# Performance work log

Hardware: AMD Instinct MI355X
Metric: run time of the kernel (lower is better)

The kernel has to match this reference:

```python
import jax, jax.numpy as jnp
import numpy as np

N_CLASSES = 12
IMG_SIZE = 512
BATCH = 8

CURV_MAX = jnp.array([1.2261, 1.1558, 1.1161, 1.1195, 2.7202, 2.3714,
                      1.7055, 3.2717, 2.6716, 5.0418, 0.4293], dtype=jnp.float32)


def setup_inputs() -> dict:
    key = jax.random.key(0)
    soft_anatomy = jax.random.normal(key, (BATCH, N_CLASSES, IMG_SIZE, IMG_SIZE), dtype=jnp.float32)
    return {"soft_anatomy": soft_anatomy}


def reference(soft_anatomy):
    nc1 = N_CLASSES - 1  # 11 layer channels
    pred_mask = soft_anatomy[:, :nc1]                      # [B, 11, H, W]
    sm = jax.nn.softmax(pred_mask, axis=2)                 # softmax over height (dim 2)
    lsm = jax.nn.log_softmax(pred_mask, axis=2)
    B, C, H, W = sm.shape

    # position mask: row index broadcast over width/channels
    pos = jnp.arange(H, dtype=sm.dtype)[None, None, :, None]  # [1,1,H,1]

    # expected layer position per column: [B, 11, W]
    layer_positions = jnp.sum(sm * pos, axis=2)

    # std deviations around layer positions: [B, 11, W]
    std_deviations = jnp.sqrt(
        jnp.sum(sm * (pos - layer_positions[:, :, None, :]) ** 2, axis=2))

    # topology violations between adjacent layers: [B, 10, W]
    topology_violations = jax.nn.relu(layer_positions[:, :-1] - layer_positions[:, 1:])

    # neighbour (continuity) diff along width: [B, 11, W-1]
    continuity_violations = jnp.abs(
        (jnp.roll(layer_positions, 1, axis=2) - layer_positions)[..., 1:])

    # curvature via depthwise conv1d with sobel [-1,0..0,1] and laplace [1,0..0,-2,0..0,1]
    # (kernel length 11, replicate pad 5 -> same width). torch conv1d is cross-correlation:
    #   first[w]  = -x[w] + x[w+10]
    #   second[w] =  x[w] - 2*x[w+5] + x[w+10]
    PAD = 5
    lpp = jnp.pad(layer_positions, ((0, 0), (0, 0), (PAD, PAD)), mode='edge')
    first_order = lpp[..., 10:] - lpp[..., :-10]
    second_order = lpp[..., :-10] - 2.0 * lpp[..., 5:-5] + lpp[..., 10:]
    curvature = second_order / jnp.power(1.0 + first_order ** 2, 1.5)
    curvature_diffs = jnp.abs(curvature) - CURV_MAX[None, :, None]  # curv_max broadcast over W

    # topological_engine_1d: new[i] = max(new[i-1], lp[i]) == cumulative max over class dim
    correct_layer_positions = jax.lax.cummax(layer_positions, axis=1)

    # cumulative mask: ones channel + cumsum over height -> [B, 12, H, W]
    cum = jnp.cumsum(sm, axis=2)
    ones = jnp.ones((B, 1, H, W), dtype=sm.dtype)
    cm = jnp.concatenate([ones, cum], axis=1)

    # topological_engine_2d: y[idx] = relu(c[idx] + y[idx-1] - 1), idx = 2..n_classes-1
    def step(carry, c):
        y = jax.nn.relu(c + carry - 1.0)
        return y, y

    _, ys = jax.lax.scan(step, cm[:, 1], jnp.moveaxis(cm[:, 2:], 1, 0))
    top_correct = jnp.concatenate([cm[:, :2], jnp.moveaxis(ys, 0, 1)], axis=1)  # [B,12,H,W]

    # separate_masks: forward diff in place; last channel unchanged
    clean_masks = jnp.concatenate(
        [top_correct[:, :-1] - top_correct[:, 1:], top_correct[:, -1:]], axis=1)

    return (lsm, correct_layer_positions, clean_masks,
            std_deviations, topology_violations, continuity_violations, curvature_diffs)
```

## Files before the change

kernel.cpp:

```cpp
#include <hip/hip_runtime.h>

#define BB 8
#define NC 12
#define NC1 11
#define HH 512
#define WW 512
#define NCH 32
#define HC 16
#define NBC (BB*NC1)

static constexpr size_t CH = (size_t)HH * WW;

static constexpr size_t OFF_LSM   = 0;
static constexpr size_t OFF_CLP   = (size_t)BB * NC1 * CH;
static constexpr size_t OFF_CLEAN = OFF_CLP + (size_t)BB * NC1 * WW;
static constexpr size_t OFF_STD   = OFF_CLEAN + (size_t)BB * NC * CH;
static constexpr size_t OFF_TOPO  = OFF_STD + (size_t)BB * NC1 * WW;
static constexpr size_t OFF_CONT  = OFF_TOPO + (size_t)BB * (NC1 - 1) * WW;
static constexpr size_t OFF_CURV  = OFF_CONT + (size_t)BB * NC1 * (WW - 1);

static constexpr size_t WS_E    = 0;
static constexpr size_t WS_P    = (size_t)NBC * NCH * WW;
static constexpr size_t WS_Q    = 2 * WS_P;
static constexpr size_t WS_INV  = 3 * WS_P;
static constexpr size_t WS_LOG  = WS_INV + (size_t)NBC * WW;
static constexpr size_t WS_LP   = WS_LOG + (size_t)NBC * WW;

__global__ __launch_bounds__(512) void k1_partials(const float* __restrict__ in,
                                                   float* __restrict__ ws) {
    const int w4 = threadIdx.x & 127;
    const int cg = threadIdx.x >> 7;
    const int chunk = blockIdx.x * 4 + cg;
    const int bc = blockIdx.y;
    const int b = bc / NC1, c = bc % NC1;

    const float* p = in + ((size_t)(b * NC + c) * HH + (size_t)chunk * HC) * WW + 4 * w4;
    float4 E = make_float4(0.f, 0.f, 0.f, 0.f);
    float4 P = E, Q = E;
#pragma unroll
    for (int i = 0; i < HC; ++i) {
        const float4 x = *(const float4*)(p + (size_t)i * WW);
        const float h = (float)(chunk * HC + i);
        const float ex = expf(x.x), ey = expf(x.y), ez = expf(x.z), ew = expf(x.w);
        E.x += ex; E.y += ey; E.z += ez; E.w += ew;
        P.x += h * ex; P.y += h * ey; P.z += h * ez; P.w += h * ew;
        Q.x += h * h * ex; Q.y += h * h * ey; Q.z += h * h * ez; Q.w += h * h * ew;
    }
    const size_t o = ((size_t)bc * NCH + chunk) * WW + 4 * w4;
    *(float4*)(ws + WS_E + o) = E;
    *(float4*)(ws + WS_P + o) = P;
    *(float4*)(ws + WS_Q + o) = Q;
}

__global__ __launch_bounds__(512) void k2_reduce(float* __restrict__ ws,
                                                 float* __restrict__ out) {
    const int w = threadIdx.x & 127;
    const int q = threadIdx.x >> 7;
    const int wt = blockIdx.x;
    const int bc = blockIdx.y;
    const int wg = wt * 128 + w;

    __shared__ float sE[4][128], sP[4][128], sQ[4][128];

    const size_t base = (size_t)bc * NCH * WW + wg;
    float e[8];
    float Es = 0.f, Ps = 0.f, Qs = 0.f;
#pragma unroll
    for (int k = 0; k < 8; ++k) {
        const int ch = q * 8 + k;
        e[k] = ws[WS_E + base + (size_t)ch * WW];
        Es += e[k];
        Ps += ws[WS_P + base + (size_t)ch * WW];
        Qs += ws[WS_Q + base + (size_t)ch * WW];
    }
    sE[q][w] = Es; sP[q][w] = Ps; sQ[q][w] = Qs;
    __syncthreads();

    const float S = sE[0][w] + sE[1][w] + sE[2][w] + sE[3][w];
    const float inv = 1.f / S;
    float pre = 0.f;
    for (int q2 = 0; q2 < q; ++q2) pre += sE[q2][w];
#pragma unroll
    for (int k = 0; k < 8; ++k) {
        const int ch = q * 8 + k;
        ws[WS_E + base + (size_t)ch * WW] = pre * inv;
        pre += e[k];
    }
    if (q == 0) {
        const float P = sP[0][w] + sP[1][w] + sP[2][w] + sP[3][w];
        const float Q = sQ[0][w] + sQ[1][w] + sQ[2][w] + sQ[3][w];
        const float lp = P * inv;
        float var = Q * inv - lp * lp;
        if (var < 0.f) var = 0.f;
        const size_t o = (size_t)bc * WW + wg;
        ws[WS_INV + o] = inv;
        ws[WS_LOG + o] = logf(S);
        ws[WS_LP + o]  = lp;
        out[OFF_STD + o] = sqrtf(var);
    }
}

__global__ __launch_bounds__(256) void k4_main(const float* __restrict__ in,
                                               const float* __restrict__ ws,
                                               float* __restrict__ out) {
    const int t = threadIdx.x;
    const int wh = blockIdx.x, chunk = blockIdx.y, b = blockIdx.z;
    const int w = wh * 256 + t;

    float cum[NC1], inv[NC1], lgs[NC1];
#pragma unroll
    for (int c = 0; c < NC1; ++c) {
        const size_t bc = (size_t)(b * NC1 + c);
        cum[c] = ws[WS_E + (bc * NCH + chunk) * WW + w];
        inv[c] = ws[WS_INV + bc * WW + w];
        lgs[c] = ws[WS_LOG + bc * WW + w];
    }

    const float* ip = in + (size_t)b * NC * CH + (size_t)(chunk * HC) * WW + w;
    float* lsm = out + OFF_LSM + (size_t)b * NC1 * CH + (size_t)(chunk * HC) * WW + w;
    float* cln = out + OFF_CLEAN + (size_t)b * NC * CH + (size_t)(chunk * HC) * WW + w;

    for (int i = 0; i < HC; ++i) {
        const size_t ho = (size_t)i * WW;
        float x[NC1];
#pragma unroll
        for (int c = 0; c < NC1; ++c)
            x[c] = ip[(size_t)c * CH + ho];
#pragma unroll
        for (int c = 0; c < NC1; ++c) {
            cum[c] += expf(x[c]) * inv[c];
            lsm[(size_t)c * CH + ho] = x[c] - lgs[c];
        }
        float tc = cum[0];
        cln[ho] = 1.f - tc;
#pragma unroll
        for (int k = 1; k < NC1; ++k) {
            const float t2 = fmaxf(cum[k] + tc - 1.f, 0.f);
            cln[(size_t)k * CH + ho] = tc - t2;
            tc = t2;
        }
        cln[(size_t)NC1 * CH + ho] = tc;
    }

    if (chunk != 0) return;
    const float CM[NC1] = {1.2261f, 1.1558f, 1.1161f, 1.1195f, 2.7202f, 2.3714f,
                           1.7055f, 3.2717f, 2.6716f, 5.0418f, 0.4293f};
    const float* lp = ws + WS_LP;
    const int wm = (w - 5 < 0) ? 0 : w - 5;
    const int wp = (w + 5 > WW - 1) ? WW - 1 : w + 5;
    float m = 0.f, prev = 0.f;
    for (int c = 0; c < NC1; ++c) {
        const size_t rb = (size_t)(b * NC1 + c) * WW;
        const float lv = lp[rb + w];
        m = (c == 0) ? lv : fmaxf(m, lv);
        out[OFF_CLP + rb + w] = m;
        if (c > 0)
            out[OFF_TOPO + (size_t)(b * (NC1 - 1) + (c - 1)) * WW + w] = fmaxf(prev - lv, 0.f);
        prev = lv;
        if (w < WW - 1) {
            const float nxt = lp[rb + w + 1];
            out[OFF_CONT + (size_t)(b * NC1 + c) * (WW - 1) + w] = fabsf(lv - nxt);
        }
        const float a  = lp[rb + wm];
        const float bb = lp[rb + wp];
        const float fo = bb - a;
        const float so = a - 2.f * lv + bb;
        const float bs = 1.f + fo * fo;
        out[OFF_CURV + rb + w] = fabsf(so / (bs * sqrtf(bs))) - CM[c];
    }
}

extern "C" void kernel_launch(void* const* d_in, const int* in_sizes, int n_in,
                              void* d_out, int out_size, void* d_ws, size_t ws_size,
                              hipStream_t stream) {
    const float* in = (const float*)d_in[0];
    float* out = (float*)d_out;
    float* ws = (float*)d_ws;

    hipLaunchKernelGGL(k1_partials, dim3(NCH / 4, NBC), dim3(512), 0, stream, in, ws);
    hipLaunchKernelGGL(k2_reduce, dim3(4, NBC), dim3(512), 0, stream, ws, out);
    hipLaunchKernelGGL(k4_main, dim3(2, NCH, BB), dim3(256), 0, stream, in, ws, out);
}
```

Baseline: 78.46 us.

## Fuse three passes into one cooperative kernel with bf16 register-cached inputs

Replaces the three-kernel sequence with a single cooperative kernel that uses grid-wide syncs between the partial-sum, reduction and output phases. The input tile is held in registers as packed bf16 so the final pass does not reread the input from global memory. The intent is to cut input traffic and launch overhead. In exchange it adds grid syncs, heavy register use with possible spills, and lower precision in the log_softmax and clean-mask outputs. The old path remains as a fallback if the cooperative launch fails.

```diff
diff --git a/kernel.cpp b/kernel.cpp
--- a/kernel.cpp
+++ b/kernel.cpp
@@ -1,4 +1,7 @@
 #include <hip/hip_runtime.h>
+#include <hip/hip_cooperative_groups.h>
+
+namespace cg = cooperative_groups;
 
 #define BB 8
 #define NC 12
@@ -12,140 +15,31 @@
 static constexpr size_t CH = (size_t)HH * WW;
 
 static constexpr size_t OFF_LSM   = 0;
-static constexpr size_t OFF_CLP   = (size_t)BB * NC1 * CH;
-static constexpr size_t OFF_CLEAN = OFF_CLP + (size_t)BB * NC1 * WW;
-static constexpr size_t OFF_STD   = OFF_CLEAN + (size_t)BB * NC * CH;
-static constexpr size_t OFF_TOPO  = OFF_STD + (size_t)BB * NC1 * WW;
-static constexpr size_t OFF_CONT  = OFF_TOPO + (size_t)BB * (NC1 - 1) * WW;
-static constexpr size_t OFF_CURV  = OFF_CONT + (size_t)BB * NC1 * (WW - 1);
-
-static constexpr size_t WS_E    = 0;
-static constexpr size_t WS_P    = (size_t)NBC * NCH * WW;
-static constexpr size_t WS_Q    = 2 * WS_P;
-static constexpr size_t WS_INV  = 3 * WS_P;
-static constexpr size_t WS_LOG  = WS_INV + (size_t)NBC * WW;
-static constexpr size_t WS_LP   = WS_LOG + (size_t)NBC * WW;
-
-__global__ __launch_bounds__(512) void k1_partials(const float* __restrict__ in,
-                                                   float* __restrict__ ws) {
-    const int w4 = threadIdx.x & 127;
-    const int cg = threadIdx.x >> 7;
-    const int chunk = blockIdx.x * 4 + cg;
-    const int bc = blockIdx.y;
-    const int b = bc / NC1, c = bc % NC1;
-
-    const float* p = in + ((size_t)(b * NC + c) * HH + (size_t)chunk * HC) * WW + 4 * w4;
-    float4 E = make_float4(0.f, 0.f, 0.f, 0.f);
-    float4 P = E, Q = E;
-#pragma unroll
-    for (int i = 0; i < HC; ++i) {
-        const float4 x = *(const float4*)(p + (size_t)i * WW);
-        const float h = (float)(chunk * HC + i);
-        const float ex = expf(x.x), ey = expf(x.y), ez = expf(x.z), ew = expf(x.w);
-        E.x += ex; E.y += ey; E.z += ez; E.w += ew;
-        P.x += h * ex; P.y += h * ey; P.z += h * ez; P.w += h * ew;
-        Q.x += h * h * ex; Q.y += h * h * ey; Q.z += h * h * ez; Q.w += h * h * ew;
-    }
-    const size_t o = ((size_t)bc * NCH + chunk) * WW + 4 * w4;
-    *(float4*)(ws + WS_E + o) = E;
-    *(float4*)(ws + WS_P + o) = P;
-    *(float4*)(ws + WS_Q + o) = Q;
-}
-
-__global__ __launch_bounds__(512) void k2_reduce(float* __restrict__ ws,
-                                                 float* __restrict__ out) {
-    const int w = threadIdx.x & 127;
-    const int q = threadIdx.x >> 7;
-    const int wt = blockIdx.x;
-    const int bc = blockIdx.y;
-    const int wg = wt * 128 + w;
-
-    __shared__ float sE[4][128], sP[4][128], sQ[4][128];
-
-    const size_t base = (size_t)bc * NCH * WW + wg;
-    float e[8];
-    float Es = 0.f, Ps = 0.f, Qs = 0.f;
-#pragma unroll
-    for (int k = 0; k < 8; ++k) {
-        const int ch = q * 8 + k;
-        e[k] = ws[WS_E + base + (size_t)ch * WW];
-        Es += e[k];
-        Ps += ws[WS_P + base + (size_t)ch * WW];
-        Qs += ws[WS_Q + base + (size_t)ch * WW];
-    }
-    sE[q][w] = Es; sP[q][w] = Ps; sQ[q][w] = Qs;
-    __syncthreads();
-
-    const float S = sE[0][w] + sE[1][w] + sE[2][w] + sE[3][w];
-    const float inv = 1.f / S;
-    float pre = 0.f;
-    for (int q2 = 0; q2 < q; ++q2) pre += sE[q2][w];
-#pragma unroll
-    for (int k = 0; k < 8; ++k) {
-        const int ch = q * 8 + k;
-        ws[WS_E + base + (size_t)ch * WW] = pre * inv;
-        pre += e[k];
-    }
-    if (q == 0) {
-        const float P = sP[0][w] + sP[1][w] + sP[2][w] + sP[3][w];
-        const float Q = sQ[0][w] + sQ[1][w] + sQ[2][w] + sQ[3][w];
-        const float lp = P * inv;
-        float var = Q * inv - lp * lp;
-        if (var < 0.f) var = 0.f;
-        const size_t o = (size_t)bc * WW + wg;
-        ws[WS_INV + o] = inv;
-        ws[WS_LOG + o] = logf(S);
-        ws[WS_LP + o]  = lp;
-        out[OFF_STD + o] = sqrtf(var);
-    }
-}
-
-__global__ __launch_bounds__(256) void k4_main(const float* __restrict__ in,
-                                               const float* __restrict__ ws,
-                                               float* __restrict__ out) {
-    const int t = threadIdx.x;
-    const int wh = blockIdx.x, chunk = blockIdx.y, b = blockIdx.z;
-    const int w = wh * 256 + t;
-
-    float cum[NC1], inv[NC1], lgs[NC1];
-#pragma unroll
-    for (int c = 0; c < NC1; ++c) {
-        const size_t bc = (size_t)(b * NC1 + c);
-        cum[c] = ws[WS_E + (bc * NCH + chunk) * WW + w];
-        inv[c] = ws[WS_INV + bc * WW + w];
-        lgs[c] = ws[WS_LOG + bc * WW + w];
-    }
-
-    const float* ip = in + (size_t)b * NC * CH + (size_t)(chunk * HC) * WW + w;
-    float* lsm = out + OFF_LSM + (size_t)b * NC1 * CH + (size_t)(chunk * HC) * WW + w;
-    float* cln = out + OFF_CLEAN + (size_t)b * NC * CH + (size_t)(chunk * HC) * WW + w;
-
-    for (int i = 0; i < HC; ++i) {
-        const size_t ho = (size_t)i * WW;
-        float x[NC1];
-#pragma unroll
-        for (int c = 0; c < NC1; ++c)
-            x[c] = ip[(size_t)c * CH + ho];
-#pragma unroll
-        for (int c = 0; c < NC1; ++c) {
-            cum[c] += expf(x[c]) * inv[c];
-            lsm[(size_t)c * CH + ho] = x[c] - lgs[c];
-        }
-        float tc = cum[0];
-        cln[ho] = 1.f - tc;
-#pragma unroll
-        for (int k = 1; k < NC1; ++k) {
-            const float t2 = fmaxf(cum[k] + tc - 1.f, 0.f);
-            cln[(size_t)k * CH + ho] = tc - t2;
-            tc = t2;
-        }
-        cln[(size_t)NC1 * CH + ho] = tc;
-    }
-
-    if (chunk != 0) return;
+static constexpr size_t OFF_CLP   = 23068672;
+static constexpr size_t OFF_CLEAN = 23113728;
+static constexpr size_t OFF_STD   = 48279552;
+static constexpr size_t OFF_TOPO  = 48324608;
+static constexpr size_t OFF_CONT  = 48365568;
+static constexpr size_t OFF_CURV  = 48410536;
+
+static constexpr size_t NE    = (size_t)NBC * NCH * WW;
+static constexpr size_t WS_E  = 0;
+static constexpr size_t WS_P  = NE;
+static constexpr size_t WS_Q  = 2 * NE;
+static constexpr size_t WS_INV = 3 * NE;
+static constexpr size_t NST   = (size_t)NBC * WW;
+static constexpr size_t WS_LOG = WS_INV + NST;
+static constexpr size_t WS_LP  = WS_LOG + NST;
+
+__device__ __forceinline__ unsigned f2bf(float f) {
+    unsigned u = __float_as_uint(f);
+    return (u + 0x7fffu + ((u >> 16) & 1u)) >> 16;
+}
+
+__device__ __forceinline__ void smalls_body(const float* __restrict__ lp,
+                                            float* __restrict__ out, int b, int w) {
     const float CM[NC1] = {1.2261f, 1.1558f, 1.1161f, 1.1195f, 2.7202f, 2.3714f,
                            1.7055f, 3.2717f, 2.6716f, 5.0418f, 0.4293f};
-    const float* lp = ws + WS_LP;
     const int wm = (w - 5 < 0) ? 0 : w - 5;
     const int wp = (w + 5 > WW - 1) ? WW - 1 : w + 5;
     float m = 0.f, prev = 0.f;
@@ -170,6 +64,235 @@
     }
 }
 
+__global__ __launch_bounds__(512) void fused_coop(const float* __restrict__ in,
+                                                  float* __restrict__ ws,
+                                                  float* __restrict__ out) {
+    cg::grid_group grid = cg::this_grid();
+    const int t = threadIdx.x;
+    const int bid = blockIdx.x;
+    const int b = bid >> 5, ck = bid & 31;
+    const int w = t;
+
+    unsigned xpk[NC1][HC / 2];
+
+#pragma unroll
+    for (int c = 0; c < NC1; ++c) {
+        const float* p = in + ((size_t)(b * NC + c) * HH + ck * HC) * WW + w;
+        float E = 0.f, P = 0.f, Q = 0.f;
+#pragma unroll
+        for (int i = 0; i < HC; ++i) {
+            const float xv = p[(size_t)i * WW];
+            const float e = expf(xv);
+            const float h = (float)(ck * HC + i);
+            E += e; P += h * e; Q += h * h * e;
+            if (i & 1) xpk[c][i >> 1] |= f2bf(xv) << 16;
+            else       xpk[c][i >> 1]  = f2bf(xv);
+        }
+        const size_t o = ((size_t)(b * NC1 + c) * NCH + ck) * WW + w;
+        ws[WS_E + o] = E; ws[WS_P + o] = P; ws[WS_Q + o] = Q;
+    }
+    __threadfence();
+    grid.sync();
+
+    {
+        const int lin = bid * 512 + t;
+        const int col = lin >> 1, q = lin & 1;
+        if (col < (int)NST) {
+            const int bc = col >> 9, w2 = col & 511;
+            const size_t cb = (size_t)bc * NCH * WW + w2;
+            float e[16];
+            float Se = 0.f, Sp = 0.f, Sq = 0.f;
+#pragma unroll
+            for (int k = 0; k < 16; ++k) {
+                const size_t oo = cb + (size_t)(q * 16 + k) * WW;
+                e[k] = ws[WS_E + oo];
+                Se += e[k];
+                Sp += ws[WS_P + oo];
+                Sq += ws[WS_Q + oo];
+            }
+            const float So = __shfl_xor(Se, 1);
+            const float Po = __shfl_xor(Sp, 1);
+            const float Qo = __shfl_xor(Sq, 1);
+            const float S = Se + So, P = Sp + Po, Q = Sq + Qo;
+            const float inv = 1.f / S;
+            float run = (q == 1) ? So : 0.f;
+#pragma unroll
+            for (int k = 0; k < 16; ++k) {
+                const size_t oo = cb + (size_t)(q * 16 + k) * WW;
+                ws[WS_E + oo] = run * inv;
+                run += e[k];
+            }
+            if (q == 0) {
+                const float lp = P * inv;
+                float var = Q * inv - lp * lp; if (var < 0.f) var = 0.f;
+                const size_t so = (size_t)bc * WW + w2;
+                ws[WS_INV + so] = inv;
+                ws[WS_LOG + so] = logf(S);
+                ws[WS_LP + so]  = lp;
+                out[OFF_STD + so] = sqrtf(var);
+            }
+        }
+    }
+    __threadfence();
+    grid.sync();
+
+    {
+        float cum[NC1], iv[NC1], lg[NC1];
+#pragma unroll
+        for (int c = 0; c < NC1; ++c) {
+            const size_t bc = (size_t)(b * NC1 + c);
+            cum[c] = ws[WS_E + (bc * NCH + ck) * WW + w];
+            iv[c]  = ws[WS_INV + bc * WW + w];
+            lg[c]  = ws[WS_LOG + bc * WW + w];
+        }
+        const size_t hb = (size_t)(ck * HC) * WW + w;
+        float* lsm = out + OFF_LSM + (size_t)b * NC1 * CH + hb;
+        float* cln = out + OFF_CLEAN + (size_t)b * NC * CH + hb;
+#pragma unroll
+        for (int i = 0; i < HC; ++i) {
+            const size_t ho = (size_t)i * WW;
+#pragma unroll
+            for (int c = 0; c < NC1; ++c) {
+                const unsigned pk = xpk[c][i >> 1];
+                const float xv = __uint_as_float((i & 1) ? (pk & 0xffff0000u) : (pk << 16));
+                lsm[(size_t)c * CH + ho] = xv - lg[c];
+                cum[c] += expf(xv) * iv[c];
+            }
+            float tc = cum[0];
+            cln[ho] = 1.f - tc;
+#pragma unroll
+            for (int k = 1; k < NC1; ++k) {
+                const float t2 = fmaxf(cum[k] + tc - 1.f, 0.f);
+                cln[(size_t)k * CH + ho] = tc - t2;
+                tc = t2;
+            }
+            cln[(size_t)NC1 * CH + ho] = tc;
+        }
+    }
+
+    if (ck == 0) smalls_body(ws + WS_LP, out, b, w);
+}
+
+__global__ __launch_bounds__(512) void k1_partials(const float* __restrict__ in,
+                                                   float* __restrict__ ws) {
+    const int w4 = threadIdx.x & 127;
+    const int cg2 = threadIdx.x >> 7;
+    const int chunk = blockIdx.x * 4 + cg2;
+    const int bc = blockIdx.y;
+    const int b = bc / NC1, c = bc % NC1;
+
+    const float* p = in + ((size_t)(b * NC + c) * HH + (size_t)chunk * HC) * WW + 4 * w4;
+    float4 E = make_float4(0.f, 0.f, 0.f, 0.f);
+    float4 P = E, Q = E;
+#pragma unroll
+    for (int i = 0; i < HC; ++i) {
+        const float4 x = *(const float4*)(p + (size_t)i * WW);
+        const float h = (float)(chunk * HC + i);
+        const float ex = expf(x.x), ey = expf(x.y), ez = expf(x.z), ew = expf(x.w);
+        E.x += ex; E.y += ey; E.z += ez; E.w += ew;
+        P.x += h * ex; P.y += h * ey; P.z += h * ez; P.w += h * ew;
+        Q.x += h * h * ex; Q.y += h * h * ey; Q.z += h * h * ez; Q.w += h * h * ew;
+    }
+    const size_t o = ((size_t)bc * NCH + chunk) * WW + 4 * w4;
+    *(float4*)(ws + WS_E + o) = E;
+    *(float4*)(ws + WS_P + o) = P;
+    *(float4*)(ws + WS_Q + o) = Q;
+}
+
+__global__ __launch_bounds__(512) void k2_reduce(float* __restrict__ ws,
+                                                 float* __restrict__ out) {
+    const int w = threadIdx.x & 127;
+    const int q = threadIdx.x >> 7;
+    const int wt = blockIdx.x;
+    const int bc = blockIdx.y;
+    const int wg = wt * 128 + w;
+
+    __shared__ float sE[4][128], sP[4][128], sQ[4][128];
+
+    const size_t base = (size_t)bc * NCH * WW + wg;
+    float e[8];
+    float Es = 0.f, Ps = 0.f, Qs = 0.f;
+#pragma unroll
+    for (int k = 0; k < 8; ++k) {
+        const int ch = q * 8 + k;
+        e[k] = ws[WS_E + base + (size_t)ch * WW];
+        Es += e[k];
+        Ps += ws[WS_P + base + (size_t)ch * WW];
+        Qs += ws[WS_Q + base + (size_t)ch * WW];
+    }
+    sE[q][w] = Es; sP[q][w] = Ps; sQ[q][w] = Qs;
+    __syncthreads();
+
+    const float S = sE[0][w] + sE[1][w] + sE[2][w] + sE[3][w];
+    const float inv = 1.f / S;
+    float pre = 0.f;
+    for (int q2 = 0; q2 < q; ++q2) pre += sE[q2][w];
+#pragma unroll
+    for (int k = 0; k < 8; ++k) {
+        const int ch = q * 8 + k;
+        ws[WS_E + base + (size_t)ch * WW] = pre * inv;
+        pre += e[k];
+    }
+    if (q == 0) {
+        const float P = sP[0][w] + sP[1][w] + sP[2][w] + sP[3][w];
+        const float Q = sQ[0][w] + sQ[1][w] + sQ[2][w] + sQ[3][w];
+        const float lp = P * inv;
+        float var = Q * inv - lp * lp;
+        if (var < 0.f) var = 0.f;
+        const size_t o = (size_t)bc * WW + wg;
+        ws[WS_INV + o] = inv;
+        ws[WS_LOG + o] = logf(S);
+        ws[WS_LP + o]  = lp;
+        out[OFF_STD + o] = sqrtf(var);
+    }
+}
+
+__global__ __launch_bounds__(256) void k4_main(const float* __restrict__ in,
+                                               const float* __restrict__ ws,
+                                               float* __restrict__ out) {
+    const int t = threadIdx.x;
+    const int wh = blockIdx.x, chunk = blockIdx.y, b = blockIdx.z;
+    const int w = wh * 256 + t;
+
+    float cum[NC1], inv[NC1], lgs[NC1];
+#pragma unroll
+    for (int c = 0; c < NC1; ++c) {
+        const size_t bc = (size_t)(b * NC1 + c);
+        cum[c] = ws[WS_E + (bc * NCH + chunk) * WW + w];
+        inv[c] = ws[WS_INV + bc * WW + w];
+        lgs[c] = ws[WS_LOG + bc * WW + w];
+    }
+
+    const float* ip = in + (size_t)b * NC * CH + (size_t)(chunk * HC) * WW + w;
+    float* lsm = out + OFF_LSM + (size_t)b * NC1 * CH + (size_t)(chunk * HC) * WW + w;
+    float* cln = out + OFF_CLEAN + (size_t)b * NC * CH + (size_t)(chunk * HC) * WW + w;
+
+    for (int i = 0; i < HC; ++i) {
+        const size_t ho = (size_t)i * WW;
+        float x[NC1];
+#pragma unroll
+        for (int c = 0; c < NC1; ++c)
+            x[c] = ip[(size_t)c * CH + ho];
+#pragma unroll
+        for (int c = 0; c < NC1; ++c) {
+            cum[c] += expf(x[c]) * inv[c];
+            lsm[(size_t)c * CH + ho] = x[c] - lgs[c];
+        }
+        float tc = cum[0];
+        cln[ho] = 1.f - tc;
+#pragma unroll
+        for (int k = 1; k < NC1; ++k) {
+            const float t2 = fmaxf(cum[k] + tc - 1.f, 0.f);
+            cln[(size_t)k * CH + ho] = tc - t2;
+            tc = t2;
+        }
+        cln[(size_t)NC1 * CH + ho] = tc;
+    }
+
+    if (chunk != 0) return;
+    smalls_body(ws + WS_LP, out, b, w);
+}
+
 extern "C" void kernel_launch(void* const* d_in, const int* in_sizes, int n_in,
                               void* d_out, int out_size, void* d_ws, size_t ws_size,
                               hipStream_t stream) {
@@ -177,7 +300,12 @@
     float* out = (float*)d_out;
     float* ws = (float*)d_ws;
 
-    hipLaunchKernelGGL(k1_partials, dim3(NCH / 4, NBC), dim3(512), 0, stream, in, ws);
-    hipLaunchKernelGGL(k2_reduce, dim3(4, NBC), dim3(512), 0, stream, ws, out);
-    hipLaunchKernelGGL(k4_main, dim3(2, NCH, BB), dim3(256), 0, stream, in, ws, out);
-}
+    void* args[] = { (void*)&in, (void*)&ws, (void*)&out };
+    hipError_t err = hipLaunchCooperativeKernel(reinterpret_cast<void*>(fused_coop),
+                                                dim3(256), dim3(512), args, 0, stream);
+    if (err != hipSuccess) {
+        hipLaunchKernelGGL(k1_partials, dim3(NCH / 4, NBC), dim3(512), 0, stream, in, ws);
+        hipLaunchKernelGGL(k2_reduce, dim3(4, NBC), dim3(512), 0, stream, ws, out);
+        hipLaunchKernelGGL(k4_main, dim3(2, NCH, BB), dim3(256), 0, stream, in, ws, out);
+    }
+}
```

Result: slower. 274.7 us (+250.1%).
